# Performance work log

Measured on AMD Instinct MI355X. Metric: run time of the kernel, lower is better.

The kernel has to match this reference:

```python
import jax, jax.numpy as jnp
import numpy as np

IN_F = 8192
OUT_F = 8192
R = 16
LORA_ALPHA = 32
BLOCK = 64
SCALING = LORA_ALPHA / R  # 2.0
NUMEL = IN_F * OUT_F


def dequantize_4bit(packed, scales):
    # packed: [numel//2] bytes (stored as int32 in [0,255]); element 2i = low nibble, 2i+1 = high nibble
    low = packed & 0xF
    high = (packed >> 4) & 0xF
    q = jnp.stack([low, high], axis=-1).reshape(-1)          # [numel] ints in [0,15]
    flat = q.astype(jnp.float32) - 8.0                        # signed 4-bit
    flat = (flat.reshape(-1, BLOCK) * scales[:, None]).reshape(-1)  # blockwise scale
    return flat.reshape(OUT_F, IN_F)


def setup_inputs() -> dict:
    key = jax.random.key(0)
    k1, k2, k3, k4, k5 = jax.random.split(key, 5)
    x = jax.random.normal(k1, (1, 64, IN_F), dtype=jnp.float32)
    packed_weights = jax.random.randint(k2, (NUMEL // 2,), 0, 256, dtype=jnp.int32)
    block_scales = jax.random.uniform(k3, (NUMEL // BLOCK,), dtype=jnp.float32) * 0.05
    # kaiming_uniform(a=sqrt(5)) on [R, IN_F] -> bound = 1/sqrt(IN_F)
    bound = 1.0 / np.sqrt(IN_F)
    lora_A = jax.random.uniform(k4, (R, IN_F), minval=-bound, maxval=bound, dtype=jnp.float32)
    # original init is zeros; use small randn for a non-trivial baseline
    lora_B = jax.random.normal(k5, (OUT_F, R), dtype=jnp.float32) * 0.02
    return {"x": x, "packed_weights": packed_weights, "block_scales": block_scales,
            "lora_A": lora_A, "lora_B": lora_B}


def reference(x, packed_weights, block_scales, lora_A, lora_B):
    W = dequantize_4bit(packed_weights, block_scales).astype(x.dtype)  # [OUT_F, IN_F]
    base_out = jnp.einsum('bsi,oi->bso', x, W)                         # no bias (bias_buffer=None)
    lora_out = jnp.einsum('bsr,or->bso', jnp.einsum('bsi,ri->bsr', x, lora_A), lora_B) * SCALING
    return base_out + lora_out
```

## Files before the change

### kernel.cpp

```cpp
#include <hip/hip_runtime.h>
#include <hip/hip_bf16.h>

#define IN_F 8192
#define OUT_F 8192
#define SEQ 64
#define LORA_R 16
#define KH 4096

typedef __attribute__((ext_vector_type(4))) float f32x4;
typedef __attribute__((ext_vector_type(4))) int i32x4;
typedef __attribute__((ext_vector_type(8))) unsigned short u16x8;
typedef __attribute__((ext_vector_type(4))) unsigned short u16x4;
typedef _Float16 f16x2 __attribute__((ext_vector_type(2)));
typedef _Float16 f16x8 __attribute__((ext_vector_type(8)));

__global__ __launch_bounds__(256) void k_prep(
    const float* __restrict__ x, const float* __restrict__ A,
    unsigned short* __restrict__ xb, float* __restrict__ t) {
    __shared__ float part[64];
    const int s = blockIdx.x;
    const int w = threadIdx.x >> 6, lane = threadIdx.x & 63;
    const int kbase = w * 2048;
    const float* xr = x + s * IN_F + kbase;

    f32x4 xv[8];
    #pragma unroll
    for (int j = 0; j < 8; ++j) {
        xv[j] = *(const f32x4*)(xr + j * 256 + lane * 4);
        u16x4 h;
        h[0] = __builtin_bit_cast(unsigned short, (_Float16)xv[j].x);
        h[1] = __builtin_bit_cast(unsigned short, (_Float16)xv[j].y);
        h[2] = __builtin_bit_cast(unsigned short, (_Float16)xv[j].z);
        h[3] = __builtin_bit_cast(unsigned short, (_Float16)xv[j].w);
        *(u16x4*)(xb + s * IN_F + kbase + j * 256 + lane * 4) = h;
    }

    float acc[LORA_R];
    #pragma unroll
    for (int r = 0; r < LORA_R; ++r) acc[r] = 0.f;
    #pragma unroll
    for (int r = 0; r < LORA_R; ++r) {
        const float* ar = A + r * IN_F + kbase;
        #pragma unroll
        for (int j = 0; j < 8; ++j) {
            f32x4 av = *(const f32x4*)(ar + j * 256 + lane * 4);
            acc[r] = fmaf(xv[j].x, av.x, acc[r]);
            acc[r] = fmaf(xv[j].y, av.y, acc[r]);
            acc[r] = fmaf(xv[j].z, av.z, acc[r]);
            acc[r] = fmaf(xv[j].w, av.w, acc[r]);
        }
    }
    #pragma unroll
    for (int r = 0; r < LORA_R; ++r) {
        float v = acc[r];
        #pragma unroll
        for (int off = 32; off; off >>= 1) v += __shfl_down(v, off, 64);
        if (lane == 0) part[w * 16 + r] = v;
    }
    __syncthreads();
    if (threadIdx.x < 16)
        t[s * LORA_R + threadIdx.x] = part[threadIdx.x] + part[16 + threadIdx.x] +
                                      part[32 + threadIdx.x] + part[48 + threadIdx.x];
}

__global__ __launch_bounds__(512, 4) void k_main(
    const int* __restrict__ packed, const float* __restrict__ scales,
    const unsigned short* __restrict__ xb, const float* __restrict__ t,
    const float* __restrict__ B, float* __restrict__ out) {
    __shared__ char lds[60928];
    _Float16* xs = (_Float16*)lds;
    int* wt = (int*)(lds + 34816);
    float* scs = (float*)(lds + 52224);
    float* accs = (float*)lds;

    const int tid = threadIdx.x;
    const int n0 = (blockIdx.x >> 1) * 32;
    const int kh = blockIdx.x & 1;
    const int w = tid >> 6, lane = tid & 63;
    const int nh = w >> 2, wkk = w & 3;
    const int q = lane >> 4, c16 = lane & 15;

    {
        int row = tid >> 4, g = tid & 15;
        f32x4 v = *(const f32x4*)(scales + (n0 + row) * (IN_F / 64) + kh * 64 + g * 4);
        *(f32x4*)(scs + row * 68 + g * 4) = v;
    }

    const int xrow = tid >> 3, xseg = tid & 7;
    const int wrow = tid >> 4, wg = tid & 15;
    const unsigned short* xsrc = xb + xrow * IN_F + kh * KH + xseg * 16;
    const int* wsrc = packed + (long)(n0 + wrow) * (IN_F / 2) + kh * (KH / 2) + wg * 4;

    f32x4 acc[4];
    #pragma unroll
    for (int mt = 0; mt < 4; ++mt) acc[mt] = (f32x4){0.f, 0.f, 0.f, 0.f};

    u16x8 gx0, gx1; i32x4 gw;
    gx0 = *(const u16x8*)(xsrc);
    gx1 = *(const u16x8*)(xsrc + 8);
    gw  = *(const i32x4*)(wsrc);
    *(u16x8*)(xs + xrow * 136 + xseg * 16)     = gx0;
    *(u16x8*)(xs + xrow * 136 + xseg * 16 + 8) = gx1;
    *(i32x4*)(wt + wrow * 68 + wg * 4)         = gw;
    __syncthreads();

    const f16x2 c1032 = {(_Float16)1032.0f, (_Float16)1032.0f};

    for (int kt = 0; kt < 32; ++kt) {
        const int cur = kt & 1;
        if (kt < 31) {
            gx0 = *(const u16x8*)(xsrc + (kt + 1) * 128);
            gx1 = *(const u16x8*)(xsrc + (kt + 1) * 128 + 8);
            gw  = *(const i32x4*)(wsrc + (kt + 1) * 64);
        }
        i32x4 pv = *(const i32x4*)(wt + cur * (32 * 68) + (nh * 16 + c16) * 68 + wkk * 16 + q * 4);
        float scf = scs[(nh * 16 + c16) * 68 + kt * 2 + (wkk >> 1)];
        _Float16 sch = (_Float16)scf;
        f16x2 sc2 = {sch, sch};
        f16x8 bf;
        #pragma unroll
        for (int m = 0; m < 4; ++m) {
            unsigned u = ((((unsigned)pv[m] << 12) | (unsigned)pv[m]) & 0x000F000Fu) | 0x64006400u;
            f16x2 h = __builtin_bit_cast(f16x2, u);
            h = (h - c1032) * sc2;
            bf[2 * m] = h.x;
            bf[2 * m + 1] = h.y;
        }
        const _Float16* xbase = xs + cur * (64 * 136) + wkk * 32 + q * 8;
        #pragma unroll
        for (int mt = 0; mt < 4; ++mt) {
            f16x8 af = *(const f16x8*)(xbase + (mt * 16 + c16) * 136);
            acc[mt] = __builtin_amdgcn_mfma_f32_16x16x32_f16(af, bf, acc[mt], 0, 0, 0);
        }
        __syncthreads();
        if (kt < 31) {
            *(u16x8*)(xs + (1 - cur) * (64 * 136) + xrow * 136 + xseg * 16)     = gx0;
            *(u16x8*)(xs + (1 - cur) * (64 * 136) + xrow * 136 + xseg * 16 + 8) = gx1;
            *(i32x4*)(wt + (1 - cur) * (32 * 68) + wrow * 68 + wg * 4)          = gw;
        }
        __syncthreads();
    }

    float* myacc = accs + w * (64 * 17);
    #pragma unroll
    for (int mt = 0; mt < 4; ++mt)
        #pragma unroll
        for (int r = 0; r < 4; ++r)
            myacc[(mt * 16 + q * 4 + r) * 17 + c16] = acc[mt][r];
    __syncthreads();

    #pragma unroll
    for (int j = 0; j < 4; ++j) {
        int p = tid + j * 512;
        int s = p >> 5, c = p & 31;
        const float* ab = accs + (c >> 4) * 4 * (64 * 17) + s * 17 + (c & 15);
        float v = ab[0] + ab[64 * 17] + ab[2 * 64 * 17] + ab[3 * 64 * 17];
        if (kh == 0) {
            const float* tp = t + s * LORA_R;
            const float* bp = B + (n0 + c) * LORA_R;
            f32x4 t0 = *(const f32x4*)tp,       t1 = *(const f32x4*)(tp + 4);
            f32x4 t2 = *(const f32x4*)(tp + 8), t3 = *(const f32x4*)(tp + 12);
            f32x4 b0 = *(const f32x4*)bp,       b1 = *(const f32x4*)(bp + 4);
            f32x4 b2 = *(const f32x4*)(bp + 8), b3 = *(const f32x4*)(bp + 12);
            float lr = t0.x * b0.x + t0.y * b0.y + t0.z * b0.z + t0.w * b0.w
                     + t1.x * b1.x + t1.y * b1.y + t1.z * b1.z + t1.w * b1.w
                     + t2.x * b2.x + t2.y * b2.y + t2.z * b2.z + t2.w * b2.w
                     + t3.x * b3.x + t3.y * b3.y + t3.z * b3.z + t3.w * b3.w;
            v += 2.0f * lr;
        }
        unsafeAtomicAdd(&out[s * OUT_F + n0 + c], v);
    }
}

extern "C" void kernel_launch(void* const* d_in, const int* in_sizes, int n_in,
                              void* d_out, int out_size, void* d_ws, size_t ws_size,
                              hipStream_t stream) {
    const float* x      = (const float*)d_in[0];
    const int* packed   = (const int*)d_in[1];
    const float* scales = (const float*)d_in[2];
    const float* lora_A = (const float*)d_in[3];
    const float* lora_B = (const float*)d_in[4];
    float* out = (float*)d_out;

    unsigned short* xb = (unsigned short*)d_ws;
    float* t = (float*)((char*)d_ws + (size_t)SEQ * IN_F * 2);

    hipMemsetAsync(out, 0, (size_t)SEQ * OUT_F * sizeof(float), stream);
    k_prep<<<SEQ, 256, 0, stream>>>(x, lora_A, xb, t);
    k_main<<<512, 512, 0, stream>>>(packed, scales, xb, t, lora_B, out);
}
```

Measured before the change: 234.4 us.

## Use direct global-to-LDS loads with XOR swizzle and a single barrier per step

Replaces register-staged global loads plus explicit LDS stores with global_load_lds DMA-style loads straight into shared memory. Padded LDS rows are replaced by an XOR swizzle to avoid bank conflicts. The two barriers per k-step become one waitcnt+barrier at the loop top. This removes VGPR staging and LDS write instructions but makes each iteration wait for the full prefetch, which limits overlap.

```diff
diff --git a/kernel.cpp b/kernel.cpp
--- a/kernel.cpp
+++ b/kernel.cpp
@@ -13,6 +13,13 @@
 typedef __attribute__((ext_vector_type(4))) unsigned short u16x4;
 typedef _Float16 f16x2 __attribute__((ext_vector_type(2)));
 typedef _Float16 f16x8 __attribute__((ext_vector_type(8)));
+
+typedef __attribute__((address_space(3))) unsigned int lds_u32;
+typedef const __attribute__((address_space(1))) unsigned int glb_u32;
+
+__device__ __forceinline__ void gl_lds16(const void* g, void* l) {
+    __builtin_amdgcn_global_load_lds((glb_u32*)g, (lds_u32*)l, 16, 0, 0);
+}
 
 __global__ __launch_bounds__(256) void k_prep(
     const float* __restrict__ x, const float* __restrict__ A,
@@ -67,10 +74,10 @@
     const int* __restrict__ packed, const float* __restrict__ scales,
     const unsigned short* __restrict__ xb, const float* __restrict__ t,
     const float* __restrict__ B, float* __restrict__ out) {
-    __shared__ char lds[60928];
+    __shared__ char lds[57856];
     _Float16* xs = (_Float16*)lds;
-    int* wt = (int*)(lds + 34816);
-    float* scs = (float*)(lds + 52224);
+    int* wt = (int*)(lds + 32768);
+    float* scs = (float*)(lds + 49152);
     float* accs = (float*)lds;
 
     const int tid = threadIdx.x;
@@ -80,41 +87,54 @@
     const int nh = w >> 2, wkk = w & 3;
     const int q = lane >> 4, c16 = lane & 15;
 
+    const int lrow = lane >> 4, lcol = lane & 15;
+    const int xr0 = w * 8 + lrow, xr1 = xr0 + 4;
+    const int wr  = w * 4 + lrow;
+    const unsigned short* xg0 = xb + (size_t)xr0 * IN_F + kh * KH + ((lcol ^ (xr0 & 7)) << 3);
+    const unsigned short* xg1 = xb + (size_t)xr1 * IN_F + kh * KH + ((lcol ^ (xr1 & 7)) << 3);
+    const int* wgp = packed + (long)(n0 + wr) * (IN_F / 2) + kh * (KH / 2) + ((lcol ^ (wr & 7)) << 2);
+
+    _Float16* xd0 = xs + w * 8 * 128;
+    _Float16* xd1 = xd0 + 4 * 128;
+    int* wd = wt + w * 256;
+
     {
         int row = tid >> 4, g = tid & 15;
         f32x4 v = *(const f32x4*)(scales + (n0 + row) * (IN_F / 64) + kh * 64 + g * 4);
         *(f32x4*)(scs + row * 68 + g * 4) = v;
     }
 
-    const int xrow = tid >> 3, xseg = tid & 7;
-    const int wrow = tid >> 4, wg = tid & 15;
-    const unsigned short* xsrc = xb + xrow * IN_F + kh * KH + xseg * 16;
-    const int* wsrc = packed + (long)(n0 + wrow) * (IN_F / 2) + kh * (KH / 2) + wg * 4;
-
     f32x4 acc[4];
     #pragma unroll
     for (int mt = 0; mt < 4; ++mt) acc[mt] = (f32x4){0.f, 0.f, 0.f, 0.f};
 
-    u16x8 gx0, gx1; i32x4 gw;
-    gx0 = *(const u16x8*)(xsrc);
-    gx1 = *(const u16x8*)(xsrc + 8);
-    gw  = *(const i32x4*)(wsrc);
-    *(u16x8*)(xs + xrow * 136 + xseg * 16)     = gx0;
-    *(u16x8*)(xs + xrow * 136 + xseg * 16 + 8) = gx1;
-    *(i32x4*)(wt + wrow * 68 + wg * 4)         = gw;
-    __syncthreads();
+    const int pvo = (nh * 16 + c16) * 64 + ((wkk * 16 + q * 4) ^ ((c16 & 7) << 2));
+    int afo[4];
+    #pragma unroll
+    for (int mt = 0; mt < 4; ++mt)
+        afo[mt] = (mt * 16 + c16) * 128 + ((wkk * 32 + q * 8) ^ ((c16 & 7) << 3));
+    const int sco = (nh * 16 + c16) * 68 + (wkk >> 1);
+
+    gl_lds16(xg0, xd0);
+    gl_lds16(xg1, xd1);
+    gl_lds16(wgp, wd);
 
     const f16x2 c1032 = {(_Float16)1032.0f, (_Float16)1032.0f};
 
     for (int kt = 0; kt < 32; ++kt) {
+        asm volatile("s_waitcnt vmcnt(0) lgkmcnt(0)" ::: "memory");
+        __builtin_amdgcn_s_barrier();
+        __builtin_amdgcn_sched_barrier(0);
         const int cur = kt & 1;
         if (kt < 31) {
-            gx0 = *(const u16x8*)(xsrc + (kt + 1) * 128);
-            gx1 = *(const u16x8*)(xsrc + (kt + 1) * 128 + 8);
-            gw  = *(const i32x4*)(wsrc + (kt + 1) * 64);
-        }
-        i32x4 pv = *(const i32x4*)(wt + cur * (32 * 68) + (nh * 16 + c16) * 68 + wkk * 16 + q * 4);
-        float scf = scs[(nh * 16 + c16) * 68 + kt * 2 + (wkk >> 1)];
+            const int nb = 1 - cur;
+            const size_t xoff = (size_t)(kt + 1) * 128;
+            gl_lds16(xg0 + xoff, xd0 + nb * 8192);
+            gl_lds16(xg1 + xoff, xd1 + nb * 8192);
+            gl_lds16(wgp + (kt + 1) * 64, wd + nb * 2048);
+        }
+        i32x4 pv = *(const i32x4*)(wt + cur * 2048 + pvo);
+        float scf = scs[sco + kt * 2];
         _Float16 sch = (_Float16)scf;
         f16x2 sc2 = {sch, sch};
         f16x8 bf;
@@ -126,20 +146,14 @@
             bf[2 * m] = h.x;
             bf[2 * m + 1] = h.y;
         }
-        const _Float16* xbase = xs + cur * (64 * 136) + wkk * 32 + q * 8;
+        const _Float16* xbase = xs + cur * 8192;
         #pragma unroll
         for (int mt = 0; mt < 4; ++mt) {
-            f16x8 af = *(const f16x8*)(xbase + (mt * 16 + c16) * 136);
+            f16x8 af = *(const f16x8*)(xbase + afo[mt]);
             acc[mt] = __builtin_amdgcn_mfma_f32_16x16x32_f16(af, bf, acc[mt], 0, 0, 0);
         }
-        __syncthreads();
-        if (kt < 31) {
-            *(u16x8*)(xs + (1 - cur) * (64 * 136) + xrow * 136 + xseg * 16)     = gx0;
-            *(u16x8*)(xs + (1 - cur) * (64 * 136) + xrow * 136 + xseg * 16 + 8) = gx1;
-            *(i32x4*)(wt + (1 - cur) * (32 * 68) + wrow * 68 + wg * 4)          = gw;
-        }
-        __syncthreads();
-    }
+    }
+    __syncthreads();
 
     float* myacc = accs + w * (64 * 17);
     #pragma unroll
```

Result: no change. 233.1 us (-0.5%).
